# Performance work log

Measured on AMD Instinct MI355X. Metric: run time of the kernel, lower is better.

Reference implementation:

```python
import jax, jax.numpy as jnp
import numpy as np

B_, H_, W_ = 4, 64, 64
D_INNER, D_STATE, DT_RANK, K = 192, 16, 6, 4
DT_MIN, DT_MAX = 0.001, 0.1


def setup_inputs() -> dict:
    key = jax.random.key(0)
    ks = jax.random.split(key, 8)
    x = jax.random.normal(ks[0], (B_, D_INNER, H_, W_), dtype=jnp.float32)
    y = jax.random.normal(ks[1], (B_, D_INNER, H_, W_), dtype=jnp.float32)
    # x_proj: 4 stacked Linear(d_inner1 -> dt_rank + 2*d_state) weights
    x_proj_weight = jax.random.normal(ks[2], (K, DT_RANK + 2 * D_STATE, D_INNER), dtype=jnp.float32) * (D_INNER ** -0.5)
    # dt_proj weights: uniform(-dt_rank^-0.5, dt_rank^-0.5)
    s = DT_RANK ** -0.5
    dt_projs_weight = jax.random.uniform(ks[3], (K, D_INNER, DT_RANK), dtype=jnp.float32, minval=-s, maxval=s)
    # dt bias init: inverse softplus of dt ~ loguniform(dt_min, dt_max)
    dt = jnp.exp(jax.random.uniform(ks[4], (K, D_INNER), dtype=jnp.float32)
                 * (np.log(DT_MAX) - np.log(DT_MIN)) + np.log(DT_MIN))
    dt = jnp.clip(dt, 1e-4, None)
    dt_projs_bias = dt + jnp.log(-jnp.expm1(-dt))
    # A_logs: log(1..N) repeated over K*d_inner channels
    A_logs = jnp.tile(jnp.log(jnp.arange(1, D_STATE + 1, dtype=jnp.float32))[None, :], (K * D_INNER, 1))
    Ds = jnp.ones((K * D_INNER,), dtype=jnp.float32)
    ln_gamma = jnp.ones((D_INNER,), dtype=jnp.float32)
    ln_beta = jnp.zeros((D_INNER,), dtype=jnp.float32)
    return {"x": x, "y": y, "x_proj_weight": x_proj_weight, "dt_projs_weight": dt_projs_weight,
            "dt_projs_bias": dt_projs_bias, "A_logs": A_logs, "Ds": Ds,
            "ln_gamma": ln_gamma, "ln_beta": ln_beta}


def _cross_scan(t):
    # (B, C, H, W) -> (B, 4, C, L): [row-major, col-major, and their reverses]
    B, C, H, W = t.shape
    a = t.reshape(B, C, H * W)
    b = jnp.swapaxes(t, 2, 3).reshape(B, C, H * W)
    s = jnp.stack([a, b], axis=1)  # (B,2,C,L)
    return jnp.concatenate([s, jnp.flip(s, axis=-1)], axis=1)  # (B,4,C,L)


def reference(x, y, x_proj_weight, dt_projs_weight, dt_projs_bias, A_logs, Ds, ln_gamma, ln_beta):
    B, C, H, W = x.shape
    L = H * W
    N = A_logs.shape[-1]
    R = dt_projs_weight.shape[-1]
    D = dt_projs_weight.shape[1]

    xs = _cross_scan(x)  # (B,K,C,L)
    ys = _cross_scan(y)  # (B,K,D,L) -- u for the scan

    x_dbl = jnp.einsum('bkdl,kcd->bkcl', xs, x_proj_weight)
    dts, Bs, Cs = x_dbl[:, :, :R], x_dbl[:, :, R:R + N], x_dbl[:, :, R + N:]
    dts = jnp.einsum('bkrl,kdr->bkdl', dts, dt_projs_weight)  # (B,K,D,L)

    delta = jax.nn.softplus(dts + dt_projs_bias.reshape(1, K, D, 1))  # (B,K,D,L)
    A = -jnp.exp(A_logs).reshape(K, D, N)  # (K,D,N)

    # selective scan over L: h_t = exp(delta_t*A)*h_{t-1} + delta_t*B_t*u_t; y_t = C_t . h_t
    u_l = jnp.moveaxis(ys, 3, 0)      # (L,B,K,D)
    d_l = jnp.moveaxis(delta, 3, 0)   # (L,B,K,D)
    B_l = jnp.moveaxis(Bs, 3, 0)      # (L,B,K,N)
    C_l = jnp.moveaxis(Cs, 3, 0)      # (L,B,K,N)

    def step(h, inp):
        u_t, d_t, b_t, c_t = inp
        dA = jnp.exp(d_t[..., None] * A)                       # (B,K,D,N)
        h = dA * h + (d_t * u_t)[..., None] * b_t[:, :, None, :]
        y_t = jnp.einsum('bkdn,bkn->bkd', h, c_t)
        return h, y_t

    h0 = jnp.zeros((B, K, D, N), dtype=jnp.float32)
    _, y_scan = jax.lax.scan(step, h0, (u_l, d_l, B_l, C_l))   # (L,B,K,D)
    out_y = jnp.moveaxis(y_scan, 0, 3) + Ds.reshape(1, K, D, 1) * ys  # (B,K,D,L)

    # cross-merge
    inv_y = jnp.flip(out_y[:, 2:4], axis=-1)                   # (B,2,D,L)
    wh_y = jnp.swapaxes(out_y[:, 1].reshape(B, D, W, H), 2, 3).reshape(B, D, L)
    invwh_y = jnp.swapaxes(inv_y[:, 1].reshape(B, D, W, H), 2, 3).reshape(B, D, L)
    ya = out_y[:, 0] + inv_y[:, 0] + wh_y + invwh_y            # (B,D,L)

    ya = jnp.swapaxes(ya, 1, 2).reshape(B, H, W, D)
    mu = jnp.mean(ya, axis=-1, keepdims=True)
    var = jnp.var(ya, axis=-1, keepdims=True)
    return (ya - mu) * jax.lax.rsqrt(var + 1e-5) * ln_gamma + ln_beta
```

## Files before the change

kernel.cpp:

```cpp
#include <hip/hip_runtime.h>
#include <hip/hip_bf16.h>

#define BB 4
#define KK 4
#define DD 192
#define NN 16
#define RR 6
#define LL 4096
#define NC 128
#define CL 32
#define C38 38

__device__ __forceinline__ float ex2(float x) {
#if __has_builtin(__builtin_amdgcn_exp2f)
  return __builtin_amdgcn_exp2f(x);
#else
  return exp2f(x);
#endif
}

__global__ __launch_bounds__(256) void k_trans(
    const float* __restrict__ x, const float* __restrict__ y,
    float* __restrict__ xT, float* __restrict__ yT)
{
  __shared__ float t0l[64 * 65];
  __shared__ float t1l[64 * 65];
  const int tid = threadIdx.x;
  const int ti = tid & 63;
  const int r4 = tid >> 6;
  const int mm0 = blockIdx.x * 2;
  const int mm1 = mm0 + 1;
  const float* s0 = (mm0 < 768 ? x + (size_t)mm0 * 4096 : y + (size_t)(mm0 - 768) * 4096);
  const float* s1 = (mm1 < 768 ? x + (size_t)mm1 * 4096 : y + (size_t)(mm1 - 768) * 4096);
  float* d0 = (mm0 < 768 ? xT + (size_t)mm0 * 4096 : yT + (size_t)(mm0 - 768) * 4096);
  float* d1 = (mm1 < 768 ? xT + (size_t)mm1 * 4096 : yT + (size_t)(mm1 - 768) * 4096);
#pragma unroll
  for (int r = r4; r < 64; r += 4) t0l[r * 65 + ti] = s0[r * 64 + ti];
#pragma unroll
  for (int r = r4; r < 64; r += 4) t1l[r * 65 + ti] = s1[r * 64 + ti];
  __syncthreads();
#pragma unroll
  for (int r = r4; r < 64; r += 4) d0[r * 64 + ti] = t0l[ti * 65 + r];
#pragma unroll
  for (int r = r4; r < 64; r += 4) d1[r * 64 + ti] = t1l[ti * 65 + r];
}

__global__ __launch_bounds__(256) void k_proj(
    const float* __restrict__ x, const float* __restrict__ y,
    const float* __restrict__ xT, const float* __restrict__ yT,
    const float* __restrict__ xpw, const float* __restrict__ dpw,
    const float* __restrict__ dpb,
    float* __restrict__ delta_ws, float* __restrict__ u_ws,
    float* __restrict__ bs_ws, float* __restrict__ cs_ws)
{
  __shared__ float xs[64 * 65];
  __shared__ float xd[38 * 65];
  const int bid = blockIdx.x;
  const int tile = bid & 63;
  const int k = (bid >> 6) & 3;
  const int b = bid >> 8;
  const int tid = threadIdx.x;
  const int ti = tid & 63;
  const int ds4 = tid >> 6;
  const int wv = __builtin_amdgcn_readfirstlane(ds4);

  const int m = (k >= 2) ? (4095 - tile * 64 - ti) : (tile * 64 + ti);
  const int tg = tile * 64 + ti;
  const size_t bkL = (size_t)(b * KK + k) * LL;

  const float* xb = ((k & 1) ? xT : x) + (size_t)b * DD * LL;

  const int c0 = (wv == 3) ? 28 : wv * 10;
  const float* Wk = xpw + (size_t)k * C38 * DD;
  float acc[10];
#pragma unroll
  for (int j = 0; j < 10; ++j) acc[j] = 0.f;

  for (int ch = 0; ch < 3; ++ch) {
    for (int r = ds4; r < 64; r += 4)
      xs[r * 65 + ti] = xb[(size_t)(ch * 64 + r) * LL + m];
    __syncthreads();
    const float* Wc = Wk + ch * 64;
#pragma unroll 8
    for (int dj = 0; dj < 64; ++dj) {
      float xv = xs[dj * 65 + ti];
#pragma unroll
      for (int j = 0; j < 10; ++j)
        acc[j] = fmaf(xv, Wc[(c0 + j) * DD + dj], acc[j]);
    }
    __syncthreads();
  }
#pragma unroll
  for (int j = 0; j < 10; ++j) xd[(c0 + j) * 65 + ti] = acc[j];
  __syncthreads();

  const float* dpwk = dpw + (size_t)k * DD * RR + (size_t)(wv * 48) * RR;
  const float* dpbk = dpb + (size_t)k * DD + wv * 48;
  float* dst = delta_ws + (bkL + tg) * DD + wv * 48;
  for (int j0 = 0; j0 < 48; j0 += 4) {
    float4 v;
    float* vp = (float*)&v;
#pragma unroll
    for (int q = 0; q < 4; ++q) {
      int jj = j0 + q;
      float s = dpbk[jj];
#pragma unroll
      for (int r = 0; r < RR; ++r)
        s = fmaf(xd[r * 65 + ti], dpwk[jj * RR + r], s);
      vp[q] = (s > 20.f) ? s : __logf(1.f + __expf(s));
    }
    *(float4*)(dst + j0) = v;
  }

  for (int idx = tid; idx < 64 * NN; idx += 256) {
    int i = idx >> 4, n = idx & 15;
    size_t row = bkL + tile * 64 + i;
    bs_ws[row * NN + n] = xd[(RR + n) * 65 + i];
    cs_ws[row * NN + n] = xd[(RR + NN + n) * 65 + i];
  }

  if (k < 2) {
    const float* yb = ((k & 1) ? yT : y) + (size_t)b * DD * LL;
    const size_t ubkL = (size_t)(b * 2 + k) * LL;
    __syncthreads();
    for (int ch = 0; ch < 3; ++ch) {
      for (int r = ds4; r < 64; r += 4)
        xs[r * 65 + ti] = yb[(size_t)(ch * 64 + r) * LL + m];
      __syncthreads();
      float* udst = u_ws + (ubkL + tg) * DD + ch * 64 + wv * 16;
#pragma unroll
      for (int j0 = 0; j0 < 16; j0 += 4) {
        float4 v;
        float* vp = (float*)&v;
#pragma unroll
        for (int q = 0; q < 4; ++q)
          vp[q] = xs[(wv * 16 + j0 + q) * 65 + ti];
        *(float4*)(udst + j0) = v;
      }
      __syncthreads();
    }
  }
}

__global__ __launch_bounds__(192) void k_scan1(
    const float* __restrict__ delta_ws, const float* __restrict__ u_ws,
    const float* __restrict__ bs_ws, const float* __restrict__ A_logs,
    float* __restrict__ cP, float* __restrict__ cS)
{
  __shared__ float Bl[CL * NN];
  const int bid = blockIdx.x;
  const int c = bid & (NC - 1);
  const int bk = bid >> 7;
  const int k = bk & 3;
  const int b = bk >> 2;
  const int d = threadIdx.x;
  if (c == NC - 1) return;
  const int t0 = c * CL;

  float A2[NN];
  const float* al = A_logs + (size_t)(k * DD + d) * NN;
#pragma unroll
  for (int n = 0; n < NN; ++n) A2[n] = -__expf(al[n]) * 1.4426950408889634f;

  const float* bsrc = bs_ws + ((size_t)bk * LL + t0) * NN;
  for (int i = threadIdx.x; i < CL * NN; i += 192) Bl[i] = bsrc[i];
  __syncthreads();

  const float* dptr = delta_ws + ((size_t)bk * LL + t0) * DD + d;
  const int rev = k >> 1;
  const float* uptr = u_ws +
      ((size_t)(b * 2 + (k & 1)) * LL + (rev ? (LL - 1 - t0) : t0)) * DD + d;
  const int ustep = rev ? -DD : DD;

  float h[NN];
#pragma unroll
  for (int n = 0; n < NN; ++n) h[n] = 0.f;
  float dsum = 0.f;
  float de0 = dptr[0], uu0 = uptr[0];
  float de1 = dptr[DD], uu1 = uptr[ustep];
#pragma unroll 2
  for (int t = 0; t < CL; ++t) {
    float de2 = dptr[(t + 2) * DD];
    float uu2 = uptr[(t + 2) * ustep];
    float du = de0 * uu0;
    dsum += de0;
    const float4* bq = (const float4*)(Bl + t * NN);
    float4 b0 = bq[0], b1 = bq[1], b2 = bq[2], b3 = bq[3];
    const float bb[16] = {b0.x,b0.y,b0.z,b0.w, b1.x,b1.y,b1.z,b1.w,
                          b2.x,b2.y,b2.z,b2.w, b3.x,b3.y,b3.z,b3.w};
#pragma unroll
    for (int n = 0; n < NN; ++n)
      h[n] = fmaf(ex2(de0 * A2[n]), h[n], du * bb[n]);
    de0 = de1; uu0 = uu1; de1 = de2; uu1 = uu2;
  }
  float* pp = cP + (((size_t)bk * NC + c) * DD + d) * NN;
  float* sp = cS + (((size_t)bk * NC + c) * DD + d) * NN;
#pragma unroll
  for (int n = 0; n < NN; ++n) { pp[n] = ex2(dsum * A2[n]); sp[n] = h[n]; }
}

__global__ __launch_bounds__(256) void k_prefix(
    float* __restrict__ cP, const float* __restrict__ cS)
{
  const int tidg = blockIdx.x * 256 + threadIdx.x;
  const int bk = tidg / (DD * NN);
  const int e = tidg - bk * (DD * NN);
  const size_t base = (size_t)bk * NC * DD * NN + e;
  const int STRIDE = DD * NN;
  float h = 0.f;
  int c = 0;
  for (; c + 4 <= NC - 1; c += 4) {
    float p0 = cP[base + (size_t)(c + 0) * STRIDE];
    float p1 = cP[base + (size_t)(c + 1) * STRIDE];
    float p2 = cP[base + (size_t)(c + 2) * STRIDE];
    float p3 = cP[base + (size_t)(c + 3) * STRIDE];
    float s0 = cS[base + (size_t)(c + 0) * STRIDE];
    float s1 = cS[base + (size_t)(c + 1) * STRIDE];
    float s2 = cS[base + (size_t)(c + 2) * STRIDE];
    float s3 = cS[base + (size_t)(c + 3) * STRIDE];
    h = fmaf(p0, h, s0); cP[base + (size_t)(c + 0) * STRIDE] = h;
    h = fmaf(p1, h, s1); cP[base + (size_t)(c + 1) * STRIDE] = h;
    h = fmaf(p2, h, s2); cP[base + (size_t)(c + 2) * STRIDE] = h;
    h = fmaf(p3, h, s3); cP[base + (size_t)(c + 3) * STRIDE] = h;
  }
  for (; c < NC - 1; ++c) {
    float p = cP[base + (size_t)c * STRIDE];
    float s = cS[base + (size_t)c * STRIDE];
    h = fmaf(p, h, s);
    cP[base + (size_t)c * STRIDE] = h;
  }
}

__global__ __launch_bounds__(192) void k_scan2(
    float* __restrict__ dy_ws,
    const float* __restrict__ u_ws,
    const float* __restrict__ bs_ws, const float* __restrict__ cs_ws,
    const float* __restrict__ A_logs, const float* __restrict__ Ds,
    const float* __restrict__ cHin)
{
  __shared__ float Bl[CL * NN];
  __shared__ float Cl2[CL * NN];
  const int bid = blockIdx.x;
  const int c = bid & (NC - 1);
  const int bk = bid >> 7;
  const int k = bk & 3;
  const int b = bk >> 2;
  const int d = threadIdx.x;
  const int t0 = c * CL;

  float A2[NN];
  const float* al = A_logs + (size_t)(k * DD + d) * NN;
#pragma unroll
  for (int n = 0; n < NN; ++n) A2[n] = -__expf(al[n]) * 1.4426950408889634f;
  const float Dkd = Ds[k * DD + d];

  float h[NN];
  if (c == 0) {
#pragma unroll
    for (int n = 0; n < NN; ++n) h[n] = 0.f;
  } else {
    const float4* hq = (const float4*)(cHin + (((size_t)bk * NC + (c - 1)) * DD + d) * NN);
    float4 h0 = hq[0], h1 = hq[1], h2 = hq[2], h3 = hq[3];
    h[0]=h0.x; h[1]=h0.y; h[2]=h0.z; h[3]=h0.w;
    h[4]=h1.x; h[5]=h1.y; h[6]=h1.z; h[7]=h1.w;
    h[8]=h2.x; h[9]=h2.y; h[10]=h2.z; h[11]=h2.w;
    h[12]=h3.x; h[13]=h3.y; h[14]=h3.z; h[15]=h3.w;
  }

  const float* bsrc = bs_ws + ((size_t)bk * LL + t0) * NN;
  const float* csrc = cs_ws + ((size_t)bk * LL + t0) * NN;
  for (int i = threadIdx.x; i < CL * NN; i += 192) {
    Bl[i] = bsrc[i];
    Cl2[i] = csrc[i];
  }
  __syncthreads();

  float* dyp = dy_ws + ((size_t)bk * LL + t0) * DD + d;
  const int rev = k >> 1;
  const float* uptr = u_ws +
      ((size_t)(b * 2 + (k & 1)) * LL + (rev ? (LL - 1 - t0) : t0)) * DD + d;
  const int ustep = rev ? -DD : DD;

  float de0 = dyp[0], uu0 = uptr[0];
  float de1 = dyp[DD], uu1 = uptr[ustep];
#pragma unroll 2
  for (int t = 0; t < CL; ++t) {
    float de2 = dyp[(t + 2) * DD];
    float uu2 = uptr[(t + 2) * ustep];
    float du = de0 * uu0;
    const float4* bq = (const float4*)(Bl + t * NN);
    const float4* cq = (const float4*)(Cl2 + t * NN);
    float4 b0 = bq[0], b1 = bq[1], b2 = bq[2], b3 = bq[3];
    float4 c0 = cq[0], c1 = cq[1], c2 = cq[2], c3 = cq[3];
    const float bb[16] = {b0.x,b0.y,b0.z,b0.w, b1.x,b1.y,b1.z,b1.w,
                          b2.x,b2.y,b2.z,b2.w, b3.x,b3.y,b3.z,b3.w};
    const float cc[16] = {c0.x,c0.y,c0.z,c0.w, c1.x,c1.y,c1.z,c1.w,
                          c2.x,c2.y,c2.z,c2.w, c3.x,c3.y,c3.z,c3.w};
    float yv = 0.f;
#pragma unroll
    for (int n = 0; n < NN; ++n) {
      h[n] = fmaf(ex2(de0 * A2[n]), h[n], du * bb[n]);
      yv = fmaf(h[n], cc[n], yv);
    }
    dyp[t * DD] = fmaf(Dkd, uu0, yv);
    de0 = de1; uu0 = uu1; de1 = de2; uu1 = uu2;
  }
}

__global__ __launch_bounds__(256) void k_comb(
    const float* __restrict__ ybuf, const float* __restrict__ gamma,
    const float* __restrict__ beta, float* __restrict__ out)
{
  const int lane = threadIdx.x & 63;
  const int gl = blockIdx.x * 4 + (threadIdx.x >> 6);
  const int b = gl >> 12;
  const int l = gl & 4095;
  const int hh = l >> 6, ww = l & 63;
  const int lt = ww * 64 + hh;
  const size_t base = (size_t)b * KK * LL * DD;
  const float* y0 = ybuf + base + (size_t)(0 * LL + l) * DD;
  const float* y1 = ybuf + base + (size_t)(1 * LL + lt) * DD;
  const float* y2 = ybuf + base + (size_t)(2 * LL + (4095 - l)) * DD;
  const float* y3 = ybuf + base + (size_t)(3 * LL + (4095 - lt)) * DD;

  float s[3];
  float sum = 0.f, sq = 0.f;
#pragma unroll
  for (int j = 0; j < 3; ++j) {
    int d = lane + j * 64;
    float v = y0[d] + y1[d] + y2[d] + y3[d];
    s[j] = v; sum += v; sq = fmaf(v, v, sq);
  }
#pragma unroll
  for (int o = 1; o < 64; o <<= 1) {
    sum += __shfl_xor(sum, o, 64);
    sq  += __shfl_xor(sq, o, 64);
  }
  const float mu = sum * (1.f / 192.f);
  const float var = sq * (1.f / 192.f) - mu * mu;
  const float inv = rsqrtf(var + 1e-5f);
  float* op = out + (size_t)gl * DD;
#pragma unroll
  for (int j = 0; j < 3; ++j) {
    int d = lane + j * 64;
    op[d] = (s[j] - mu) * inv * gamma[d] + beta[d];
  }
}

extern "C" void kernel_launch(void* const* d_in, const int* in_sizes, int n_in,
                              void* d_out, int out_size, void* d_ws, size_t ws_size,
                              hipStream_t stream) {
  const float* x     = (const float*)d_in[0];
  const float* y     = (const float*)d_in[1];
  const float* xpw   = (const float*)d_in[2];
  const float* dpw   = (const float*)d_in[3];
  const float* dpb   = (const float*)d_in[4];
  const float* alogs = (const float*)d_in[5];
  const float* ds    = (const float*)d_in[6];
  const float* gamma = (const float*)d_in[7];
  const float* beta  = (const float*)d_in[8];
  float* w = (float*)d_ws;

  float* delta = w;
  float* u     = w + 12582912;
  float* bs    = w + 18874368;
  float* cs    = w + 19922944;
  float* cP    = w + 20971520;
  float* cS    = w + 27262976;
  float* xT    = cP;
  float* yT    = cP + 3145728;

  k_trans<<<768, 256, 0, stream>>>(x, y, xT, yT);
  k_proj<<<1024, 256, 0, stream>>>(x, y, xT, yT, xpw, dpw, dpb, delta, u, bs, cs);
  k_scan1<<<2048, 192, 0, stream>>>(delta, u, bs, alogs, cP, cS);
  k_prefix<<<192, 256, 0, stream>>>(cP, cS);
  k_scan2<<<2048, 192, 0, stream>>>(delta, u, bs, cs, alogs, ds, cP);
  k_comb<<<4096, 256, 0, stream>>>(delta, gamma, beta, (float*)d_out);
}
```

Baseline: 263.8 us.

## Split scan state across thread pairs, double chunk length, coalesce proj stores

The scan kernels now give each (d) channel two threads, each holding 8 of the 16 state elements, and combine the y contribution with a lane shuffle. Chunk length doubles to 64 with half as many chunks. k_proj now transposes delta and u through shared memory so global stores are coalesced along d rather than per-row float4 writes. The aim is more parallelism and fewer live registers in the sequential scans plus better store coalescing. The cost is extra shuffles, more barriers in k_proj, and longer sequential chunks.

```diff
diff --git a/kernel.cpp b/kernel.cpp
--- a/kernel.cpp
+++ b/kernel.cpp
@@ -7,8 +7,8 @@
 #define NN 16
 #define RR 6
 #define LL 4096
-#define NC 128
-#define CL 32
+#define NC 64
+#define CL 64
 #define C38 38
 
 __device__ __forceinline__ float ex2(float x) {
@@ -46,8 +46,8 @@
 }
 
 __global__ __launch_bounds__(256) void k_proj(
-    const float* __restrict__ x, const float* __restrict__ y,
-    const float* __restrict__ xT, const float* __restrict__ yT,
+    const float* __restrict__ x, const float* __restrict__ xT,
+    const float* __restrict__ y, const float* __restrict__ yT,
     const float* __restrict__ xpw, const float* __restrict__ dpw,
     const float* __restrict__ dpb,
     float* __restrict__ delta_ws, float* __restrict__ u_ws,
@@ -65,9 +65,8 @@
   const int wv = __builtin_amdgcn_readfirstlane(ds4);
 
   const int m = (k >= 2) ? (4095 - tile * 64 - ti) : (tile * 64 + ti);
-  const int tg = tile * 64 + ti;
   const size_t bkL = (size_t)(b * KK + k) * LL;
-
+  const size_t rowbase = bkL + tile * 64;
   const float* xb = ((k & 1) ? xT : x) + (size_t)b * DD * LL;
 
   const int c0 = (wv == 3) ? 28 : wv * 10;
@@ -75,7 +74,6 @@
   float acc[10];
 #pragma unroll
   for (int j = 0; j < 10; ++j) acc[j] = 0.f;
-
   for (int ch = 0; ch < 3; ++ch) {
     for (int r = ds4; r < 64; r += 4)
       xs[r * 65 + ti] = xb[(size_t)(ch * 64 + r) * LL + m];
@@ -94,55 +92,57 @@
   for (int j = 0; j < 10; ++j) xd[(c0 + j) * 65 + ti] = acc[j];
   __syncthreads();
 
-  const float* dpwk = dpw + (size_t)k * DD * RR + (size_t)(wv * 48) * RR;
-  const float* dpbk = dpb + (size_t)k * DD + wv * 48;
-  float* dst = delta_ws + (bkL + tg) * DD + wv * 48;
-  for (int j0 = 0; j0 < 48; j0 += 4) {
-    float4 v;
-    float* vp = (float*)&v;
-#pragma unroll
-    for (int q = 0; q < 4; ++q) {
-      int jj = j0 + q;
-      float s = dpbk[jj];
-#pragma unroll
-      for (int r = 0; r < RR; ++r)
-        s = fmaf(xd[r * 65 + ti], dpwk[jj * RR + r], s);
-      vp[q] = (s > 20.f) ? s : __logf(1.f + __expf(s));
-    }
-    *(float4*)(dst + j0) = v;
-  }
-
   for (int idx = tid; idx < 64 * NN; idx += 256) {
     int i = idx >> 4, n = idx & 15;
-    size_t row = bkL + tile * 64 + i;
+    size_t row = rowbase + i;
     bs_ws[row * NN + n] = xd[(RR + n) * 65 + i];
     cs_ws[row * NN + n] = xd[(RR + NN + n) * 65 + i];
   }
 
+  const float* dpwk = dpw + (size_t)k * DD * RR;
+  const float* dpbk = dpb + (size_t)k * DD;
+  for (int ch = 0; ch < 3; ++ch) {
+    float v[16];
+#pragma unroll
+    for (int q = 0; q < 16; ++q) {
+      const int dd2 = ch * 64 + wv * 16 + q;
+      float s = dpbk[dd2];
+#pragma unroll
+      for (int r = 0; r < RR; ++r)
+        s = fmaf(xd[r * 65 + ti], dpwk[dd2 * RR + r], s);
+      v[q] = (s > 20.f) ? s : __logf(1.f + __expf(s));
+    }
+    __syncthreads();
+#pragma unroll
+    for (int q = 0; q < 16; ++q) xs[ti * 65 + wv * 16 + q] = v[q];
+    __syncthreads();
+    float* dbase = delta_ws + rowbase * DD + ch * 64;
+#pragma unroll
+    for (int it = 0; it < 16; ++it) {
+      const int i = it * 4 + ds4;
+      dbase[(size_t)i * DD + ti] = xs[i * 65 + ti];
+    }
+  }
+
   if (k < 2) {
     const float* yb = ((k & 1) ? yT : y) + (size_t)b * DD * LL;
-    const size_t ubkL = (size_t)(b * 2 + k) * LL;
-    __syncthreads();
+    const size_t urowbase = (size_t)(b * 2 + k) * LL + tile * 64;
     for (int ch = 0; ch < 3; ++ch) {
+      __syncthreads();
       for (int r = ds4; r < 64; r += 4)
         xs[r * 65 + ti] = yb[(size_t)(ch * 64 + r) * LL + m];
       __syncthreads();
-      float* udst = u_ws + (ubkL + tg) * DD + ch * 64 + wv * 16;
-#pragma unroll
-      for (int j0 = 0; j0 < 16; j0 += 4) {
-        float4 v;
-        float* vp = (float*)&v;
-#pragma unroll
-        for (int q = 0; q < 4; ++q)
-          vp[q] = xs[(wv * 16 + j0 + q) * 65 + ti];
-        *(float4*)(udst + j0) = v;
+      float* ubase = u_ws + urowbase * DD + ch * 64;
+#pragma unroll
+      for (int it = 0; it < 16; ++it) {
+        const int i = it * 4 + ds4;
+        ubase[(size_t)i * DD + ti] = xs[ti * 65 + i];
       }
-      __syncthreads();
-    }
-  }
-}
-
-__global__ __launch_bounds__(192) void k_scan1(
+    }
+  }
+}
+
+__global__ __launch_bounds__(384) void k_scan1(
     const float* __restrict__ delta_ws, const float* __restrict__ u_ws,
     const float* __restrict__ bs_ws, const float* __restrict__ A_logs,
     float* __restrict__ cP, float* __restrict__ cS)
@@ -150,20 +150,21 @@
   __shared__ float Bl[CL * NN];
   const int bid = blockIdx.x;
   const int c = bid & (NC - 1);
-  const int bk = bid >> 7;
+  const int bk = bid >> 6;
   const int k = bk & 3;
   const int b = bk >> 2;
-  const int d = threadIdx.x;
+  const int tid = threadIdx.x;
+  const int d = tid >> 1, nh = tid & 1;
   if (c == NC - 1) return;
   const int t0 = c * CL;
 
-  float A2[NN];
-  const float* al = A_logs + (size_t)(k * DD + d) * NN;
-#pragma unroll
-  for (int n = 0; n < NN; ++n) A2[n] = -__expf(al[n]) * 1.4426950408889634f;
+  float A2[8];
+  const float* al = A_logs + (size_t)(k * DD + d) * NN + nh * 8;
+#pragma unroll
+  for (int n = 0; n < 8; ++n) A2[n] = -__expf(al[n]) * 1.4426950408889634f;
 
   const float* bsrc = bs_ws + ((size_t)bk * LL + t0) * NN;
-  for (int i = threadIdx.x; i < CL * NN; i += 192) Bl[i] = bsrc[i];
+  for (int i = tid; i < CL * NN; i += 384) Bl[i] = bsrc[i];
   __syncthreads();
 
   const float* dptr = delta_ws + ((size_t)bk * LL + t0) * DD + d;
@@ -172,9 +173,9 @@
       ((size_t)(b * 2 + (k & 1)) * LL + (rev ? (LL - 1 - t0) : t0)) * DD + d;
   const int ustep = rev ? -DD : DD;
 
-  float h[NN];
-#pragma unroll
-  for (int n = 0; n < NN; ++n) h[n] = 0.f;
+  float h[8];
+#pragma unroll
+  for (int n = 0; n < 8; ++n) h[n] = 0.f;
   float dsum = 0.f;
   float de0 = dptr[0], uu0 = uptr[0];
   float de1 = dptr[DD], uu1 = uptr[ustep];
@@ -184,19 +185,18 @@
     float uu2 = uptr[(t + 2) * ustep];
     float du = de0 * uu0;
     dsum += de0;
-    const float4* bq = (const float4*)(Bl + t * NN);
-    float4 b0 = bq[0], b1 = bq[1], b2 = bq[2], b3 = bq[3];
-    const float bb[16] = {b0.x,b0.y,b0.z,b0.w, b1.x,b1.y,b1.z,b1.w,
-                          b2.x,b2.y,b2.z,b2.w, b3.x,b3.y,b3.z,b3.w};
-#pragma unroll
-    for (int n = 0; n < NN; ++n)
+    const float4* bq = (const float4*)(Bl + t * NN + nh * 8);
+    float4 b0 = bq[0], b1 = bq[1];
+    const float bb[8] = {b0.x,b0.y,b0.z,b0.w, b1.x,b1.y,b1.z,b1.w};
+#pragma unroll
+    for (int n = 0; n < 8; ++n)
       h[n] = fmaf(ex2(de0 * A2[n]), h[n], du * bb[n]);
     de0 = de1; uu0 = uu1; de1 = de2; uu1 = uu2;
   }
-  float* pp = cP + (((size_t)bk * NC + c) * DD + d) * NN;
-  float* sp = cS + (((size_t)bk * NC + c) * DD + d) * NN;
-#pragma unroll
-  for (int n = 0; n < NN; ++n) { pp[n] = ex2(dsum * A2[n]); sp[n] = h[n]; }
+  float* pp = cP + (((size_t)bk * NC + c) * DD + d) * NN + nh * 8;
+  float* sp = cS + (((size_t)bk * NC + c) * DD + d) * NN + nh * 8;
+#pragma unroll
+  for (int n = 0; n < 8; ++n) { pp[n] = ex2(dsum * A2[n]); sp[n] = h[n]; }
 }
 
 __global__ __launch_bounds__(256) void k_prefix(
@@ -231,7 +231,7 @@
   }
 }
 
-__global__ __launch_bounds__(192) void k_scan2(
+__global__ __launch_bounds__(384) void k_scan2(
     float* __restrict__ dy_ws,
     const float* __restrict__ u_ws,
     const float* __restrict__ bs_ws, const float* __restrict__ cs_ws,
@@ -242,34 +242,34 @@
   __shared__ float Cl2[CL * NN];
   const int bid = blockIdx.x;
   const int c = bid & (NC - 1);
-  const int bk = bid >> 7;
+  const int bk = bid >> 6;
   const int k = bk & 3;
   const int b = bk >> 2;
-  const int d = threadIdx.x;
+  const int tid = threadIdx.x;
+  const int d = tid >> 1, nh = tid & 1;
   const int t0 = c * CL;
 
-  float A2[NN];
-  const float* al = A_logs + (size_t)(k * DD + d) * NN;
-#pragma unroll
-  for (int n = 0; n < NN; ++n) A2[n] = -__expf(al[n]) * 1.4426950408889634f;
+  float A2[8];
+  const float* al = A_logs + (size_t)(k * DD + d) * NN + nh * 8;
+#pragma unroll
+  for (int n = 0; n < 8; ++n) A2[n] = -__expf(al[n]) * 1.4426950408889634f;
   const float Dkd = Ds[k * DD + d];
 
-  float h[NN];
+  float h[8];
   if (c == 0) {
 #pragma unroll
-    for (int n = 0; n < NN; ++n) h[n] = 0.f;
+    for (int n = 0; n < 8; ++n) h[n] = 0.f;
   } else {
-    const float4* hq = (const float4*)(cHin + (((size_t)bk * NC + (c - 1)) * DD + d) * NN);
-    float4 h0 = hq[0], h1 = hq[1], h2 = hq[2], h3 = hq[3];
+    const float4* hq = (const float4*)(cHin +
+        (((size_t)bk * NC + (c - 1)) * DD + d) * NN + nh * 8);
+    float4 h0 = hq[0], h1 = hq[1];
     h[0]=h0.x; h[1]=h0.y; h[2]=h0.z; h[3]=h0.w;
     h[4]=h1.x; h[5]=h1.y; h[6]=h1.z; h[7]=h1.w;
-    h[8]=h2.x; h[9]=h2.y; h[10]=h2.z; h[11]=h2.w;
-    h[12]=h3.x; h[13]=h3.y; h[14]=h3.z; h[15]=h3.w;
   }
 
   const float* bsrc = bs_ws + ((size_t)bk * LL + t0) * NN;
   const float* csrc = cs_ws + ((size_t)bk * LL + t0) * NN;
-  for (int i = threadIdx.x; i < CL * NN; i += 192) {
+  for (int i = tid; i < CL * NN; i += 384) {
     Bl[i] = bsrc[i];
     Cl2[i] = csrc[i];
   }
@@ -288,21 +288,20 @@
     float de2 = dyp[(t + 2) * DD];
     float uu2 = uptr[(t + 2) * ustep];
     float du = de0 * uu0;
-    const float4* bq = (const float4*)(Bl + t * NN);
-    const float4* cq = (const float4*)(Cl2 + t * NN);
-    float4 b0 = bq[0], b1 = bq[1], b2 = bq[2], b3 = bq[3];
-    float4 c0 = cq[0], c1 = cq[1], c2 = cq[2], c3 = cq[3];
-    const float bb[16] = {b0.x,b0.y,b0.z,b0.w, b1.x,b1.y,b1.z,b1.w,
-                          b2.x,b2.y,b2.z,b2.w, b3.x,b3.y,b3.z,b3.w};
-    const float cc[16] = {c0.x,c0.y,c0.z,c0.w, c1.x,c1.y,c1.z,c1.w,
-                          c2.x,c2.y,c2.z,c2.w, c3.x,c3.y,c3.z,c3.w};
+    const float4* bq = (const float4*)(Bl + t * NN + nh * 8);
+    const float4* cq = (const float4*)(Cl2 + t * NN + nh * 8);
+    float4 b0 = bq[0], b1 = bq[1];
+    float4 c0 = cq[0], c1 = cq[1];
+    const float bb[8] = {b0.x,b0.y,b0.z,b0.w, b1.x,b1.y,b1.z,b1.w};
+    const float cc[8] = {c0.x,c0.y,c0.z,c0.w, c1.x,c1.y,c1.z,c1.w};
     float yv = 0.f;
 #pragma unroll
-    for (int n = 0; n < NN; ++n) {
+    for (int n = 0; n < 8; ++n) {
       h[n] = fmaf(ex2(de0 * A2[n]), h[n], du * bb[n]);
       yv = fmaf(h[n], cc[n], yv);
     }
-    dyp[t * DD] = fmaf(Dkd, uu0, yv);
+    yv += __shfl_xor(yv, 1, 64);
+    if (nh == 0) dyp[t * DD] = fmaf(Dkd, uu0, yv);
     de0 = de1; uu0 = uu1; de1 = de2; uu1 = uu2;
   }
 }
@@ -366,14 +365,14 @@
   float* bs    = w + 18874368;
   float* cs    = w + 19922944;
   float* cP    = w + 20971520;
-  float* cS    = w + 27262976;
+  float* cS    = w + 24117248;
   float* xT    = cP;
-  float* yT    = cP + 3145728;
+  float* yT    = cS;
 
   k_trans<<<768, 256, 0, stream>>>(x, y, xT, yT);
-  k_proj<<<1024, 256, 0, stream>>>(x, y, xT, yT, xpw, dpw, dpb, delta, u, bs, cs);
-  k_scan1<<<2048, 192, 0, stream>>>(delta, u, bs, alogs, cP, cS);
+  k_proj<<<1024, 256, 0, stream>>>(x, xT, y, yT, xpw, dpw, dpb, delta, u, bs, cs);
+  k_scan1<<<1024, 384, 0, stream>>>(delta, u, bs, alogs, cP, cS);
   k_prefix<<<192, 256, 0, stream>>>(cP, cS);
-  k_scan2<<<2048, 192, 0, stream>>>(delta, u, bs, cs, alogs, ds, cP);
+  k_scan2<<<1024, 384, 0, stream>>>(delta, u, bs, cs, alogs, ds, cP);
   k_comb<<<4096, 256, 0, stream>>>(delta, gamma, beta, (float*)d_out);
 }
```

Result: faster. 239.1 us (-9.4%).
